# Performance work log

Measured on AMD Instinct MI355X. Metric: run time of the kernel, lower is better.

The kernel has to match this reference:

```python
import jax, jax.numpy as jnp
import numpy as np

TEMP = 0.07   # config['temperature']
EPS = 1e-8    # torch cosine-similarity eps
NEG_INF = -1e30


def _l2norm(x):
    return x / jnp.maximum(jnp.linalg.norm(x, axis=-1, keepdims=True), EPS)


def _remove_diag(m):
    # [n,n] -> [n,n-1], drop the diagonal of each row (extract_non_diagonal_matrix)
    n = m.shape[0]
    return m.reshape(-1)[:-1].reshape(n - 1, n + 1)[:, 1:].reshape(n, n - 1)


def _contrastive(e1, e2):
    # NT-Xent between two views, compared across the batch at matched temporal
    # positions (finegrain=False path). e1, e2: [b, s, d]
    b = e1.shape[0]
    z = jnp.concatenate([e1.transpose(1, 0, 2), e2.transpose(1, 0, 2)], axis=1)  # [s, 2b, d]
    zn = _l2norm(z)
    sim = jnp.einsum('pnd,pmd->pnm', zn, zn) / TEMP  # [s, 2b, 2b]
    pos = jnp.concatenate([
        jnp.diagonal(sim, b, axis1=-2, axis2=-1),
        jnp.diagonal(sim, -b, axis1=-2, axis2=-1),
    ], axis=1)  # [s, 2b]
    N = 2 * b
    eyeb = jnp.eye(b, dtype=bool)
    excl = jnp.eye(N, dtype=bool)
    excl = excl.at[:b, b:].set(excl[:b, b:] | eyeb).at[b:, :b].set(excl[b:, :b] | eyeb)
    neg = jnp.where(~excl, sim, NEG_INF)  # [s, 2b, 2b], 2b-2 live entries/row
    logits = jnp.concatenate([pos[..., None], neg], axis=-1)
    # CrossEntropyLoss(label=0), mean
    return jnp.mean(jax.nn.logsumexp(logits, axis=-1) - pos)


def _coarse_temporal(f):
    # samples within a sequence = positives, other sequences = negatives
    b, s, d = f.shape
    zn = _l2norm(f.reshape(b * s, d))
    sim = (zn @ zn.T) / TEMP  # [bs, bs]
    # diagonal over the batch blocks -> [b, s, s]
    sim_ii = jnp.diagonal(sim.reshape(b, s, b, s), axis1=0, axis2=2).transpose(2, 0, 1)
    pos = jax.vmap(_remove_diag)(sim_ii).reshape(b * s, s - 1)
    blk = jnp.repeat(jnp.repeat(~jnp.eye(b, dtype=bool), s, axis=0), s, axis=1)
    neg = jnp.where(blk, sim, NEG_INF)  # (b-1)*s live entries per row
    logits = jnp.concatenate([pos, neg], axis=1)
    return jnp.mean(jax.nn.logsumexp(logits, axis=1) - logits[:, 0])


def _ortho(x1, x2):
    # CosineEmbeddingLoss with target=-1, margin=0: mean(relu(cos(x1, x2)))
    a = _l2norm(x1.reshape(-1, x1.shape[-1]))
    b = _l2norm(x2.reshape(-1, x2.shape[-1]))
    return jnp.mean(jax.nn.relu(jnp.sum(a * b, axis=-1)))


def _forward(mod1_v1, mod1_v2, mod2_v1, mod2_v2, seq_len):
    d = mod1_v1.shape[-1]
    h = d // 2
    f1 = [mod1_v1.reshape(-1, seq_len, d), mod2_v1.reshape(-1, seq_len, d)]  # view 1, per mod
    f2 = [mod1_v2.reshape(-1, seq_len, d), mod2_v2.reshape(-1, seq_len, d)]  # view 2, per mod
    sh = lambda x: x[..., :h]
    pv = lambda x: x[..., h:]

    # (2) shared contrastive between modalities, per view
    shared_loss = _contrastive(sh(f1[0]), sh(f1[1])) + _contrastive(sh(f2[0]), sh(f2[1]))
    # (3) private contrastive between views, per modality
    private_loss = _contrastive(pv(f1[0]), pv(f2[0])) + _contrastive(pv(f1[1]), pv(f2[1]))
    # (4) orthogonality: shared-vs-private per mod per view, private-vs-private per view
    ortho_loss = (_ortho(sh(f1[0]), pv(f1[0])) + _ortho(sh(f1[1]), pv(f1[1]))
                  + _ortho(sh(f2[0]), pv(f2[0])) + _ortho(sh(f2[1]), pv(f2[1]))
                  + _ortho(pv(f1[0]), pv(f1[1])) + _ortho(pv(f2[0]), pv(f2[1])))
    # (5) temporal consistency: coarse temporal contrastive per mod per view
    temporal_loss = (_coarse_temporal(f1[0]) + _coarse_temporal(f1[1])
                     + _coarse_temporal(f2[0]) + _coarse_temporal(f2[1]))
    return shared_loss + private_loss + ortho_loss + temporal_loss


def setup_inputs() -> dict:
    key = jax.random.key(0)
    ks = jax.random.split(key, 4)
    B, S, D = 512, 8, 128
    return {
        'mod1_v1': jax.random.normal(ks[0], (B * S, D), dtype=jnp.float32),
        'mod1_v2': jax.random.normal(ks[1], (B * S, D), dtype=jnp.float32),
        'mod2_v1': jax.random.normal(ks[2], (B * S, D), dtype=jnp.float32),
        'mod2_v2': jax.random.normal(ks[3], (B * S, D), dtype=jnp.float32),
        'seq_len': S,
    }


def reference(mod1_v1, mod1_v2, mod2_v1, mod2_v2, seq_len):
    return _forward(mod1_v1, mod1_v2, mod2_v1, mod2_v2, seq_len)
```

## Files before the change

kernel.cpp:

```cpp
#include <hip/hip_runtime.h>
#include <math.h>

#define CTR_L1 0
#define CTR_L2 2048
#define RS_T   49152
#define RS_C   65536
#define SLOT   98304
#define ZF_BYTE 397312
#define ZH_BYTE 4591616

#define INV_T 14.285714285714286f
#define C1EXP 20.609929155556627f
#define EPS_N 1e-8f
#define NBLK_TAIL 192

typedef __attribute__((ext_vector_type(8))) short short8;
typedef __attribute__((ext_vector_type(4))) float floatx4;

__device__ __forceinline__ const float* pick4(const float* a, const float* b,
                                              const float* c, const float* d, int i) {
    return i == 0 ? a : i == 1 ? b : i == 2 ? c : d;
}

__device__ __forceinline__ unsigned short f2bf(float x) {
    unsigned u = __float_as_uint(x);
    u += 0x7fff + ((u >> 16) & 1);
    return (unsigned short)(u >> 16);
}

__device__ __forceinline__ ushort4 cvt4(float4 x, float sc) {
    ushort4 o;
    o.x = f2bf(x.x * sc); o.y = f2bf(x.y * sc); o.z = f2bf(x.z * sc); o.w = f2bf(x.w * sc);
    return o;
}

__global__ __launch_bounds__(256) void k_prep(const float* __restrict__ in0, const float* __restrict__ in1,
                                              const float* __restrict__ in2, const float* __restrict__ in3,
                                              float* __restrict__ ws) {
    __shared__ float ivf[128], ivs[128], ivp[128];
    __shared__ float buf[4][8][128];
    __shared__ float iv[3][32];
    __shared__ float red[3];
    const int tid = threadIdx.x;
    const int blk = blockIdx.x;

    if (blk < 128) {
        const int input = blk >> 5, g = blk & 31;
        const float* src = pick4(in0, in1, in2, in3, input) + (size_t)(g * 128) * 128;
        {
            int r = tid >> 1, half = tid & 1;
            const float* rp_ = src + r * 128 + half * 64;
            float ss = 0.0f;
            #pragma unroll
            for (int k = 0; k < 16; k++) {
                float4 x = *(const float4*)(rp_ + k * 4);
                ss = fmaf(x.x, x.x, fmaf(x.y, x.y, fmaf(x.z, x.z, fmaf(x.w, x.w, ss))));
            }
            float other = __shfl_xor(ss, 1);
            if (half == 0) {
                ivs[r] = 1.0f / fmaxf(sqrtf(ss), EPS_N);
                ivf[r] = 1.0f / fmaxf(sqrtf(ss + other), EPS_N);
            } else {
                ivp[r] = 1.0f / fmaxf(sqrtf(ss), EPS_N);
            }
        }
        __syncthreads();
        unsigned short* zf = (unsigned short*)((char*)ws + ZF_BYTE) + (size_t)input * 524288 + (size_t)g * 16384;
        unsigned short* zh = (unsigned short*)((char*)ws + ZH_BYTE) + (size_t)input * 524288;
        #pragma unroll
        for (int k = 0; k < 8; k++) {
            int ch = k * 256 + tid;
            int lr = ((ch >> 8) << 4) | (ch & 15);
            int kc = (ch >> 4) & 15;
            const float* sp = src + lr * 128 + kc * 8;
            float sc = ivf[lr];
            *(ushort4*)(zf + ch * 8)     = cvt4(*(const float4*)sp, sc);
            *(ushort4*)(zf + ch * 8 + 4) = cvt4(*(const float4*)(sp + 4), sc);
        }
        #pragma unroll
        for (int k = 0; k < 8; k++) {
            int ch = k * 256 + tid;
            int p = ch >> 8, kc = (ch >> 4) & 15, slot = ch & 15;
            int lr = slot * 8 + p;
            const float* sp = src + lr * 128 + kc * 8;
            float sc = (kc < 8 ? ivs : ivp)[lr];
            unsigned short* dst = zh + (size_t)p * 65536 + (size_t)g * 2048 + (ch & 255) * 8;
            *(ushort4*)dst       = cvt4(*(const float4*)sp, sc);
            *(ushort4*)(dst + 4) = cvt4(*(const float4*)(sp + 4), sc);
        }
        return;
    }

    const int s = blk - 128;
    int gid = s * 256 + tid;
    if (gid < 2080) ws[gid] = 0.0f;
    if (gid < 50176) ws[RS_T + gid] = 0.0f;
    if (tid < 3) red[tid] = 0.0f;

    #pragma unroll
    for (int i = 0; i < 4; i++) {
        int e4 = tid + i * 256;
        int inp = e4 >> 8, row = (e4 >> 5) & 7, c4 = e4 & 31;
        float4 f = *(const float4*)(pick4(in0, in1, in2, in3, inp) + (size_t)(s * 8 + row) * 128 + c4 * 4);
        *(float4*)(&buf[inp][row][c4 * 4]) = f;
    }
    __syncthreads();
    {
        int row32 = tid >> 3, seg = tid & 7;
        const float* rp_ = &buf[row32 >> 3][row32 & 7][seg * 16];
        float ss = 0.0f;
        #pragma unroll
        for (int k = 0; k < 4; k++) {
            float4 x = *(const float4*)(rp_ + k * 4);
            ss = fmaf(x.x, x.x, fmaf(x.y, x.y, fmaf(x.z, x.z, fmaf(x.w, x.w, ss))));
        }
        ss += __shfl_xor(ss, 1); ss += __shfl_xor(ss, 2);
        float cross = __shfl_xor(ss, 4);
        if (seg == 0) {
            iv[0][row32] = 1.0f / fmaxf(sqrtf(ss), EPS_N);
            iv[2][row32] = 1.0f / fmaxf(sqrtf(ss + cross), EPS_N);
        }
        if (seg == 4) iv[1][row32] = 1.0f / fmaxf(sqrtf(ss), EPS_N);
    }
    __syncthreads();

    float val = 0.0f;
    int cat = -1;
    if (tid < 48) {
        const int oa[6]  = {0, 2, 1, 3, 0, 1};
        const int oaf[6] = {0, 0, 0, 0, 64, 64};
        const int ob[6]  = {0, 2, 1, 3, 2, 3};
        int term = tid >> 3, row = tid & 7;
        const float* A = &buf[oa[term]][row][oaf[term]];
        const float* B = &buf[ob[term]][row][64];
        float d = 0.0f;
        #pragma unroll
        for (int k = 0; k < 16; k++) {
            float4 x = *(const float4*)(A + k * 4);
            float4 y = *(const float4*)(B + k * 4);
            d = fmaf(x.x, y.x, fmaf(x.y, y.y, fmaf(x.z, y.z, fmaf(x.w, y.w, d))));
        }
        float ia = iv[oaf[term] ? 1 : 0][oa[term] * 8 + row];
        float ib = iv[1][ob[term] * 8 + row];
        val = fmaxf(d * ia * ib, 0.0f);
        cat = 2;
    } else if (tid < 80) {
        const int ca[4] = {0, 1, 0, 2}, cb[4] = {2, 3, 1, 3}, coff[4] = {0, 0, 64, 64};
        int call = (tid - 48) >> 3, row = (tid - 48) & 7;
        const float* A = &buf[ca[call]][row][coff[call]];
        const float* B = &buf[cb[call]][row][coff[call]];
        float d = 0.0f;
        #pragma unroll
        for (int k = 0; k < 16; k++) {
            float4 x = *(const float4*)(A + k * 4);
            float4 y = *(const float4*)(B + k * 4);
            d = fmaf(x.x, y.x, fmaf(x.y, y.y, fmaf(x.z, y.z, fmaf(x.w, y.w, d))));
        }
        int ivb = coff[call] ? 1 : 0;
        val = d * iv[ivb][ca[call] * 8 + row] * iv[ivb][cb[call] * 8 + row];
        cat = 0;
    } else if (tid < 136) {
        int u = tid - 80;
        int inp = u / 14, v = u % 14, pp = v >> 1, half = v & 1;
        int ra = (pp == 0) ? 1 : (pp + 1);
        const float* A = &buf[inp][ra][half * 64];
        const float* B = &buf[inp][0][half * 64];
        float d = 0.0f;
        #pragma unroll
        for (int k = 0; k < 16; k++) {
            float4 x = *(const float4*)(A + k * 4);
            float4 y = *(const float4*)(B + k * 4);
            d = fmaf(x.x, y.x, fmaf(x.y, y.y, fmaf(x.z, y.z, fmaf(x.w, y.w, d))));
        }
        float wgt = (pp == 0) ? 2.0f : 1.0f;
        val = d * wgt * iv[2][inp * 8 + ra] * iv[2][inp * 8];
        cat = 1;
    }
    if (cat >= 0) atomicAdd(&red[cat], val);
    __syncthreads();
    if (tid == 0) atomicAdd(ws + SLOT + 32 * 24, red[0]);
    if (tid == 1) atomicAdd(ws + SLOT + 32 * 25, red[1]);
    if (tid == 2) atomicAdd(ws + SLOT + 32 * (16 + (s & 7)), red[2]);
}

__global__ __launch_bounds__(256, 3) void k_gram(float* __restrict__ ws) {
    const int tid = threadIdx.x;
    const int b = blockIdx.x;
    const int w = tid >> 6, lane = tid & 63, quad = (tid >> 4) & 3, l15 = tid & 15;
    const int wrow = (w >> 1) * 64, wcol = (w & 1) * 64;
    const int laneoff = (lane >> 4) * 128 + (lane & 15) * 8;

    const short* aPtr;
    const short* planeA;
    const short* planeB;
    int nk, ntiles, jbase, modm;
    float* rsR;
    float* rsCbase;
    bool temporal = (b < 1024);
    int rt;

    if (temporal) {
        int input = b >> 8;
        rt = (b >> 3) & 31;
        int chunk = b & 7;
        const short* zf = (const short*)((const char*)ws + ZF_BYTE) + (size_t)input * 524288;
        planeA = planeB = zf;
        aPtr = zf + (rt * 8 + (wrow >> 4)) * 2048 + laneoff;
        nk = 2; modm = 31;
        jbase = chunk * 2;
        ntiles = 2 + ((chunk == 7 && rt < 16) ? 1 : 0);
        rsR = ws + RS_T + input * 4096 + rt * 128;
        rsCbase = ws + RS_T + input * 4096;
    } else {
        int c = b - 1024;
        int call = c >> 6, p = (c >> 3) & 7;
        rt = c & 7;
        const int ca[4] = {0, 1, 0, 2}, cb[4] = {2, 3, 1, 3};
        const int hb = (call >= 2) ? 8 : 0;
        const short* zh = (const short*)((const char*)ws + ZH_BYTE);
        planeA = zh + (size_t)ca[call] * 524288 + (size_t)p * 65536 + hb * 128;
        planeB = zh + (size_t)cb[call] * 524288 + (size_t)p * 65536 + hb * 128;
        const short* rpl = (rt < 4) ? planeA : planeB;
        aPtr = rpl + ((rt & 3) * 8 + (wrow >> 4)) * 2048 + laneoff;
        nk = 1; modm = 7;
        jbase = 0;
        ntiles = (rt < 4) ? 5 : 4;
        rsR = ws + RS_C + (call * 8 + p) * 1024 + rt * 128;
        rsCbase = ws + RS_C + (call * 8 + p) * 1024;
    }

    float rp_acc[16];
    #pragma unroll
    for (int i = 0; i < 16; i++) rp_acc[i] = 0.0f;

    for (int t = 0; t < ntiles; t++) {
        int j = (temporal && t == 2) ? 16 : (jbase + t);
        int ct = (rt + j) & modm;
        bool diag = (j == 0);
        const short* bPtr;
        if (temporal) {
            bPtr = planeA + (ct * 8 + (wcol >> 4)) * 2048 + laneoff;
        } else {
            const short* cpl = (ct < 4) ? planeA : planeB;
            bPtr = cpl + ((ct & 3) * 8 + (wcol >> 4)) * 2048 + laneoff;
        }

        floatx4 acc[4][4];
        #pragma unroll
        for (int ri = 0; ri < 4; ri++)
            #pragma unroll
            for (int ci = 0; ci < 4; ci++) acc[ri][ci] = (floatx4){0.f, 0.f, 0.f, 0.f};

        for (int ksb = 0; ksb < 2 * nk; ksb++) {
            const int koff = ksb * 512;
            short8 a[4], bb[4];
            #pragma unroll
            for (int i = 0; i < 4; i++) {
                a[i]  = *(const short8*)(aPtr + i * 2048 + koff);
                bb[i] = *(const short8*)(bPtr + i * 2048 + koff);
            }
            #pragma unroll
            for (int ri = 0; ri < 4; ri++)
                #pragma unroll
                for (int ci = 0; ci < 4; ci++)
                    acc[ri][ci] = __builtin_amdgcn_mfma_f32_16x16x32_bf16(a[ri], bb[ci], acc[ri][ci], 0, 0, 0);
        }

        if (diag) {
            #pragma unroll
            for (int ri = 0; ri < 4; ri++) {
                #pragma unroll
                for (int reg = 0; reg < 4; reg++) {
                    int rloc = wrow + ri * 16 + quad * 4 + reg;
                    float rp = 0.f;
                    #pragma unroll
                    for (int ci = 0; ci < 4; ci++) {
                        int cloc = wcol + ci * 16 + l15;
                        float ex = __builtin_amdgcn_exp2f(fmaf(acc[ri][ci][reg], C1EXP, -C1EXP));
                        rp += (cloc != rloc) ? ex : 0.f;
                    }
                    rp_acc[ri * 4 + reg] += rp;
                }
            }
        } else {
            float colp[4] = {0.f, 0.f, 0.f, 0.f};
            #pragma unroll
            for (int ri = 0; ri < 4; ri++) {
                #pragma unroll
                for (int reg = 0; reg < 4; reg++) {
                    float rp = 0.f;
                    #pragma unroll
                    for (int ci = 0; ci < 4; ci++) {
                        float ex = __builtin_amdgcn_exp2f(fmaf(acc[ri][ci][reg], C1EXP, -C1EXP));
                        rp += ex;
                        colp[ci] += ex;
                    }
                    rp_acc[ri * 4 + reg] += rp;
                }
            }
            float* rsC = rsCbase + ct * 128;
            #pragma unroll
            for (int ci = 0; ci < 4; ci++) {
                colp[ci] += __shfl_xor(colp[ci], 16);
                colp[ci] += __shfl_xor(colp[ci], 32);
                if (lane < 16) atomicAdd(rsC + wcol + ci * 16 + l15, colp[ci]);
            }
        }
    }

    #pragma unroll
    for (int ri = 0; ri < 4; ri++) {
        #pragma unroll
        for (int reg = 0; reg < 4; reg++) {
            float rp = rp_acc[ri * 4 + reg];
            rp += __shfl_xor(rp, 1); rp += __shfl_xor(rp, 2);
            rp += __shfl_xor(rp, 4); rp += __shfl_xor(rp, 8);
            if (l15 == 0) atomicAdd(rsR + wrow + ri * 16 + quad * 4 + reg, rp);
        }
    }
}

__global__ __launch_bounds__(256) void k_tail(float* __restrict__ ws, float* __restrict__ out) {
    __shared__ float tred[4];
    __shared__ int lastf;
    const int tid = threadIdx.x;
    const int b = blockIdx.x;
    const int idx = b * 256 + tid;

    float l = __logf(ws[RS_T + idx]);
    #pragma unroll
    for (int m = 1; m < 64; m <<= 1) l += __shfl_xor(l, m);
    if ((tid & 63) == 0) tred[tid >> 6] = l;
    __syncthreads();
    if (tid == 0) {
        float bs = tred[0] + tred[1] + tred[2] + tred[3];
        int slot = (idx < 16384) ? (8 + (b & 7)) : (b & 7);
        atomicAdd(ws + SLOT + 32 * slot, bs);
    }
    __syncthreads();
    if (tid == 0) {
        int last = 0;
        int o1 = __hip_atomic_fetch_add((int*)(ws + CTR_L1 + 32 * (b & 7)), 1,
                                        __ATOMIC_RELAXED, __HIP_MEMORY_SCOPE_AGENT);
        if (o1 == 23) {
            int o2 = __hip_atomic_fetch_add((int*)(ws + CTR_L2), 1,
                                            __ATOMIC_RELAXED, __HIP_MEMORY_SCOPE_AGENT);
            last = (o2 == 7);
        }
        lastf = last;
    }
    __syncthreads();
    if (!lastf) return;

    if (tid < 64) {
        float v2 = 0.0f;
        if (tid < 26) {
            float x = __hip_atomic_load(ws + SLOT + 32 * tid, __ATOMIC_RELAXED, __HIP_MEMORY_SCOPE_AGENT);
            float wgt;
            if (tid < 8)       wgt = 1.0f / 8192.0f;
            else if (tid < 24) wgt = 1.0f / 4096.0f;
            else if (tid == 24) wgt = -2.0f * INV_T / 8192.0f;
            else                wgt = -INV_T / 4096.0f;
            v2 = x * wgt;
        }
        #pragma unroll
        for (int m = 1; m < 64; m <<= 1) v2 += __shfl_xor(v2, m);
        if (tid == 0) out[0] = v2 + 8.0f * INV_T;
    }
}

extern "C" void kernel_launch(void* const* d_in, const int* in_sizes, int n_in,
                              void* d_out, int out_size, void* d_ws, size_t ws_size,
                              hipStream_t stream) {
    (void)in_sizes; (void)n_in; (void)out_size; (void)ws_size;
    const float* in0 = (const float*)d_in[0];
    const float* in1 = (const float*)d_in[1];
    const float* in2 = (const float*)d_in[2];
    const float* in3 = (const float*)d_in[3];
    float* ws = (float*)d_ws;
    float* out = (float*)d_out;

    hipLaunchKernelGGL(k_prep, dim3(640), dim3(256), 0, stream, in0, in1, in2, in3, ws);
    hipLaunchKernelGGL(k_gram, dim3(1280), dim3(256), 0, stream, ws);
    hipLaunchKernelGGL(k_tail, dim3(NBLK_TAIL), dim3(256), 0, stream, ws, out);
}
```

Baseline: 114.3 us.

## Keep A fragments in registers and give each temporal block twice as many tiles

```diff
diff --git a/kernel.cpp b/kernel.cpp
--- a/kernel.cpp
+++ b/kernel.cpp
@@ -190,133 +190,188 @@
     const int wrow = (w >> 1) * 64, wcol = (w & 1) * 64;
     const int laneoff = (lane >> 4) * 128 + (lane & 15) * 8;
 
-    const short* aPtr;
-    const short* planeA;
-    const short* planeB;
-    int nk, ntiles, jbase, modm;
-    float* rsR;
-    float* rsCbase;
-    bool temporal = (b < 1024);
-    int rt;
-
-    if (temporal) {
-        int input = b >> 8;
-        rt = (b >> 3) & 31;
-        int chunk = b & 7;
+    float rp_acc[16];
+    #pragma unroll
+    for (int i = 0; i < 16; i++) rp_acc[i] = 0.0f;
+
+    if (b < 512) {
+        const int input = b >> 7, rt = (b >> 2) & 31, chunk = b & 3;
         const short* zf = (const short*)((const char*)ws + ZF_BYTE) + (size_t)input * 524288;
-        planeA = planeB = zf;
-        aPtr = zf + (rt * 8 + (wrow >> 4)) * 2048 + laneoff;
-        nk = 2; modm = 31;
-        jbase = chunk * 2;
-        ntiles = 2 + ((chunk == 7 && rt < 16) ? 1 : 0);
-        rsR = ws + RS_T + input * 4096 + rt * 128;
-        rsCbase = ws + RS_T + input * 4096;
+        const short* aPtr = zf + (rt * 8 + (wrow >> 4)) * 2048 + laneoff;
+        float* rsR = ws + RS_T + input * 4096 + rt * 128;
+        float* rsCbase = ws + RS_T + input * 4096;
+
+        short8 A[16];
+        #pragma unroll
+        for (int ksb = 0; ksb < 4; ksb++)
+            #pragma unroll
+            for (int i = 0; i < 4; i++)
+                A[ksb * 4 + i] = *(const short8*)(aPtr + i * 2048 + ksb * 512);
+
+        const int ntiles = 4 + ((chunk == 3 && rt < 16) ? 1 : 0);
+        for (int t = 0; t < ntiles; t++) {
+            int j = (t == 4) ? 16 : (chunk * 4 + t);
+            int ct = (rt + j) & 31;
+            const short* bPtr = zf + (ct * 8 + (wcol >> 4)) * 2048 + laneoff;
+
+            floatx4 acc[4][4];
+            #pragma unroll
+            for (int ri = 0; ri < 4; ri++)
+                #pragma unroll
+                for (int ci = 0; ci < 4; ci++) acc[ri][ci] = (floatx4){0.f, 0.f, 0.f, 0.f};
+
+            #pragma unroll
+            for (int ksb = 0; ksb < 4; ksb++) {
+                short8 bb[4];
+                #pragma unroll
+                for (int i = 0; i < 4; i++) bb[i] = *(const short8*)(bPtr + i * 2048 + ksb * 512);
+                #pragma unroll
+                for (int ri = 0; ri < 4; ri++)
+                    #pragma unroll
+                    for (int ci = 0; ci < 4; ci++)
+                        acc[ri][ci] = __builtin_amdgcn_mfma_f32_16x16x32_bf16(A[ksb * 4 + ri], bb[ci], acc[ri][ci], 0, 0, 0);
+            }
+
+            if (j == 0) {
+                #pragma unroll
+                for (int ri = 0; ri < 4; ri++)
+                    #pragma unroll
+                    for (int reg = 0; reg < 4; reg++) {
+                        int rloc = wrow + ri * 16 + quad * 4 + reg;
+                        float rp = 0.f;
+                        #pragma unroll
+                        for (int ci = 0; ci < 4; ci++) {
+                            int cloc = wcol + ci * 16 + l15;
+                            float ex = __builtin_amdgcn_exp2f(fmaf(acc[ri][ci][reg], C1EXP, -C1EXP));
+                            rp += (cloc != rloc) ? ex : 0.f;
+                        }
+                        rp_acc[ri * 4 + reg] += rp;
+                    }
+            } else {
+                float colp[4] = {0.f, 0.f, 0.f, 0.f};
+                #pragma unroll
+                for (int ri = 0; ri < 4; ri++)
+                    #pragma unroll
+                    for (int reg = 0; reg < 4; reg++) {
+                        float rp = 0.f;
+                        #pragma unroll
+                        for (int ci = 0; ci < 4; ci++) {
+                            float ex = __builtin_amdgcn_exp2f(fmaf(acc[ri][ci][reg], C1EXP, -C1EXP));
+                            rp += ex;
+                            colp[ci] += ex;
+                        }
+                        rp_acc[ri * 4 + reg] += rp;
+                    }
+                float* rsC = rsCbase + ct * 128;
+                #pragma unroll
+                for (int ci = 0; ci < 4; ci++) {
+                    colp[ci] += __shfl_xor(colp[ci], 16);
+                    colp[ci] += __shfl_xor(colp[ci], 32);
+                    if (lane < 16) atomicAdd(rsC + wcol + ci * 16 + l15, colp[ci]);
+                }
+            }
+        }
+        #pragma unroll
+        for (int ri = 0; ri < 4; ri++)
+            #pragma unroll
+            for (int reg = 0; reg < 4; reg++) {
+                float rp = rp_acc[ri * 4 + reg];
+                rp += __shfl_xor(rp, 1); rp += __shfl_xor(rp, 2);
+                rp += __shfl_xor(rp, 4); rp += __shfl_xor(rp, 8);
+                if (l15 == 0) atomicAdd(rsR + wrow + ri * 16 + quad * 4 + reg, rp);
+            }
     } else {
-        int c = b - 1024;
-        int call = c >> 6, p = (c >> 3) & 7;
-        rt = c & 7;
+        const int c = b - 512;
+        const int call = c >> 6, p = (c >> 3) & 7, rt = c & 7;
         const int ca[4] = {0, 1, 0, 2}, cb[4] = {2, 3, 1, 3};
         const int hb = (call >= 2) ? 8 : 0;
         const short* zh = (const short*)((const char*)ws + ZH_BYTE);
-        planeA = zh + (size_t)ca[call] * 524288 + (size_t)p * 65536 + hb * 128;
-        planeB = zh + (size_t)cb[call] * 524288 + (size_t)p * 65536 + hb * 128;
+        const short* planeA = zh + (size_t)ca[call] * 524288 + (size_t)p * 65536 + hb * 128;
+        const short* planeB = zh + (size_t)cb[call] * 524288 + (size_t)p * 65536 + hb * 128;
         const short* rpl = (rt < 4) ? planeA : planeB;
-        aPtr = rpl + ((rt & 3) * 8 + (wrow >> 4)) * 2048 + laneoff;
-        nk = 1; modm = 7;
-        jbase = 0;
-        ntiles = (rt < 4) ? 5 : 4;
-        rsR = ws + RS_C + (call * 8 + p) * 1024 + rt * 128;
-        rsCbase = ws + RS_C + (call * 8 + p) * 1024;
-    }
-
-    float rp_acc[16];
-    #pragma unroll
-    for (int i = 0; i < 16; i++) rp_acc[i] = 0.0f;
-
-    for (int t = 0; t < ntiles; t++) {
-        int j = (temporal && t == 2) ? 16 : (jbase + t);
-        int ct = (rt + j) & modm;
-        bool diag = (j == 0);
-        const short* bPtr;
-        if (temporal) {
-            bPtr = planeA + (ct * 8 + (wcol >> 4)) * 2048 + laneoff;
-        } else {
+        const short* aPtr = rpl + ((rt & 3) * 8 + (wrow >> 4)) * 2048 + laneoff;
+        float* rsR = ws + RS_C + (call * 8 + p) * 1024 + rt * 128;
+        float* rsCbase = ws + RS_C + (call * 8 + p) * 1024;
+
+        short8 A[8];
+        #pragma unroll
+        for (int ksb = 0; ksb < 2; ksb++)
+            #pragma unroll
+            for (int i = 0; i < 4; i++)
+                A[ksb * 4 + i] = *(const short8*)(aPtr + i * 2048 + ksb * 512);
+
+        const int ntiles = 4 + ((rt < 4) ? 1 : 0);
+        for (int t = 0; t < ntiles; t++) {
+            int ct = (rt + t) & 7;
             const short* cpl = (ct < 4) ? planeA : planeB;
-            bPtr = cpl + ((ct & 3) * 8 + (wcol >> 4)) * 2048 + laneoff;
-        }
-
-        floatx4 acc[4][4];
+            const short* bPtr = cpl + ((ct & 3) * 8 + (wcol >> 4)) * 2048 + laneoff;
+
+            floatx4 acc[4][4];
+            #pragma unroll
+            for (int ri = 0; ri < 4; ri++)
+                #pragma unroll
+                for (int ci = 0; ci < 4; ci++) acc[ri][ci] = (floatx4){0.f, 0.f, 0.f, 0.f};
+
+            #pragma unroll
+            for (int ksb = 0; ksb < 2; ksb++) {
+                short8 bb[4];
+                #pragma unroll
+                for (int i = 0; i < 4; i++) bb[i] = *(const short8*)(bPtr + i * 2048 + ksb * 512);
+                #pragma unroll
+                for (int ri = 0; ri < 4; ri++)
+                    #pragma unroll
+                    for (int ci = 0; ci < 4; ci++)
+                        acc[ri][ci] = __builtin_amdgcn_mfma_f32_16x16x32_bf16(A[ksb * 4 + ri], bb[ci], acc[ri][ci], 0, 0, 0);
+            }
+
+            if (t == 0) {
+                #pragma unroll
+                for (int ri = 0; ri < 4; ri++)
+                    #pragma unroll
+                    for (int reg = 0; reg < 4; reg++) {
+                        int rloc = wrow + ri * 16 + quad * 4 + reg;
+                        float rp = 0.f;
+                        #pragma unroll
+                        for (int ci = 0; ci < 4; ci++) {
+                            int cloc = wcol + ci * 16 + l15;
+                            float ex = __builtin_amdgcn_exp2f(fmaf(acc[ri][ci][reg], C1EXP, -C1EXP));
+                            rp += (cloc != rloc) ? ex : 0.f;
+                        }
+                        rp_acc[ri * 4 + reg] += rp;
+                    }
+            } else {
+                float colp[4] = {0.f, 0.f, 0.f, 0.f};
+                #pragma unroll
+                for (int ri = 0; ri < 4; ri++)
+                    #pragma unroll
+                    for (int reg = 0; reg < 4; reg++) {
+                        float rp = 0.f;
+                        #pragma unroll
+                        for (int ci = 0; ci < 4; ci++) {
+                            float ex = __builtin_amdgcn_exp2f(fmaf(acc[ri][ci][reg], C1EXP, -C1EXP));
+                            rp += ex;
+                            colp[ci] += ex;
+                        }
+                        rp_acc[ri * 4 + reg] += rp;
+                    }
+                float* rsC = rsCbase + ct * 128;
+                #pragma unroll
+                for (int ci = 0; ci < 4; ci++) {
+                    colp[ci] += __shfl_xor(colp[ci], 16);
+                    colp[ci] += __shfl_xor(colp[ci], 32);
+                    if (lane < 16) atomicAdd(rsC + wcol + ci * 16 + l15, colp[ci]);
+                }
+            }
+        }
         #pragma unroll
         for (int ri = 0; ri < 4; ri++)
             #pragma unroll
-            for (int ci = 0; ci < 4; ci++) acc[ri][ci] = (floatx4){0.f, 0.f, 0.f, 0.f};
-
-        for (int ksb = 0; ksb < 2 * nk; ksb++) {
-            const int koff = ksb * 512;
-            short8 a[4], bb[4];
-            #pragma unroll
-            for (int i = 0; i < 4; i++) {
-                a[i]  = *(const short8*)(aPtr + i * 2048 + koff);
-                bb[i] = *(const short8*)(bPtr + i * 2048 + koff);
-            }
-            #pragma unroll
-            for (int ri = 0; ri < 4; ri++)
-                #pragma unroll
-                for (int ci = 0; ci < 4; ci++)
-                    acc[ri][ci] = __builtin_amdgcn_mfma_f32_16x16x32_bf16(a[ri], bb[ci], acc[ri][ci], 0, 0, 0);
-        }
-
-        if (diag) {
-            #pragma unroll
-            for (int ri = 0; ri < 4; ri++) {
-                #pragma unroll
-                for (int reg = 0; reg < 4; reg++) {
-                    int rloc = wrow + ri * 16 + quad * 4 + reg;
-                    float rp = 0.f;
-                    #pragma unroll
-                    for (int ci = 0; ci < 4; ci++) {
-                        int cloc = wcol + ci * 16 + l15;
-                        float ex = __builtin_amdgcn_exp2f(fmaf(acc[ri][ci][reg], C1EXP, -C1EXP));
-                        rp += (cloc != rloc) ? ex : 0.f;
-                    }
-                    rp_acc[ri * 4 + reg] += rp;
-                }
-            }
-        } else {
-            float colp[4] = {0.f, 0.f, 0.f, 0.f};
-            #pragma unroll
-            for (int ri = 0; ri < 4; ri++) {
-                #pragma unroll
-                for (int reg = 0; reg < 4; reg++) {
-                    float rp = 0.f;
-                    #pragma unroll
-                    for (int ci = 0; ci < 4; ci++) {
-                        float ex = __builtin_amdgcn_exp2f(fmaf(acc[ri][ci][reg], C1EXP, -C1EXP));
-                        rp += ex;
-                        colp[ci] += ex;
-                    }
-                    rp_acc[ri * 4 + reg] += rp;
-                }
-            }
-            float* rsC = rsCbase + ct * 128;
-            #pragma unroll
-            for (int ci = 0; ci < 4; ci++) {
-                colp[ci] += __shfl_xor(colp[ci], 16);
-                colp[ci] += __shfl_xor(colp[ci], 32);
-                if (lane < 16) atomicAdd(rsC + wcol + ci * 16 + l15, colp[ci]);
-            }
-        }
-    }
-
-    #pragma unroll
-    for (int ri = 0; ri < 4; ri++) {
-        #pragma unroll
-        for (int reg = 0; reg < 4; reg++) {
-            float rp = rp_acc[ri * 4 + reg];
-            rp += __shfl_xor(rp, 1); rp += __shfl_xor(rp, 2);
-            rp += __shfl_xor(rp, 4); rp += __shfl_xor(rp, 8);
-            if (l15 == 0) atomicAdd(rsR + wrow + ri * 16 + quad * 4 + reg, rp);
-        }
+            for (int reg = 0; reg < 4; reg++) {
+                float rp = rp_acc[ri * 4 + reg];
+                rp += __shfl_xor(rp, 1); rp += __shfl_xor(rp, 2);
+                rp += __shfl_xor(rp, 4); rp += __shfl_xor(rp, 8);
+                if (l15 == 0) atomicAdd(rsR + wrow + ri * 16 + quad * 4 + reg, rp);
+            }
     }
 }
 
@@ -381,6 +436,6 @@
     float* out = (float*)d_out;
 
     hipLaunchKernelGGL(k_prep, dim3(640), dim3(256), 0, stream, in0, in1, in2, in3, ws);
-    hipLaunchKernelGGL(k_gram, dim3(1280), dim3(256), 0, stream, ws);
+    hipLaunchKernelGGL(k_gram, dim3(768), dim3(256), 0, stream, ws);
     hipLaunchKernelGGL(k_tail, dim3(NBLK_TAIL), dim3(256), 0, stream, ws, out);
 }
```

After: 124.4 us. +8.9%, slower.

## Quantize normalized embeddings to FP8 e4m3 and use FP8 MFMA for Gram tiles

Applied to the files above, without the earlier changes.

```diff
diff --git a/kernel.cpp b/kernel.cpp
--- a/kernel.cpp
+++ b/kernel.cpp
@@ -7,14 +7,13 @@
 #define RS_C   65536
 #define SLOT   98304
 #define ZF_BYTE 397312
-#define ZH_BYTE 4591616
+#define ZH8_BYTE 2494464
 
 #define INV_T 14.285714285714286f
 #define C1EXP 20.609929155556627f
 #define EPS_N 1e-8f
 #define NBLK_TAIL 192
 
-typedef __attribute__((ext_vector_type(8))) short short8;
 typedef __attribute__((ext_vector_type(4))) float floatx4;
 
 __device__ __forceinline__ const float* pick4(const float* a, const float* b,
@@ -22,16 +21,24 @@
     return i == 0 ? a : i == 1 ? b : i == 2 ? c : d;
 }
 
-__device__ __forceinline__ unsigned short f2bf(float x) {
+__device__ __forceinline__ unsigned f2e4m3(float x) {
     unsigned u = __float_as_uint(x);
-    u += 0x7fff + ((u >> 16) & 1);
-    return (unsigned short)(u >> 16);
-}
-
-__device__ __forceinline__ ushort4 cvt4(float4 x, float sc) {
-    ushort4 o;
-    o.x = f2bf(x.x * sc); o.y = f2bf(x.y * sc); o.z = f2bf(x.z * sc); o.w = f2bf(x.w * sc);
-    return o;
+    unsigned s = (u >> 24) & 0x80;
+    u &= 0x7fffffffu;
+    if (u >= 0x43e00000u) return s | 0x7e;
+    if (u < 0x3c800000u) {
+        int m = (int)rintf(__uint_as_float(u) * 512.0f);
+        return s | (unsigned)m;
+    }
+    unsigned r = u + 0x7ffffu + ((u >> 20) & 1u);
+    int e = (int)((r >> 23) & 0xffu) - 127;
+    if (e > 8) return s | 0x7e;
+    return s | (unsigned)(((e + 7) << 3) | ((r >> 20) & 7u));
+}
+
+__device__ __forceinline__ unsigned pack4_e4m3(const float* p, float sc) {
+    return f2e4m3(p[0] * sc) | (f2e4m3(p[1] * sc) << 8)
+         | (f2e4m3(p[2] * sc) << 16) | (f2e4m3(p[3] * sc) << 24);
 }
 
 __global__ __launch_bounds__(256) void k_prep(const float* __restrict__ in0, const float* __restrict__ in1,
@@ -65,28 +72,34 @@
             }
         }
         __syncthreads();
-        unsigned short* zf = (unsigned short*)((char*)ws + ZF_BYTE) + (size_t)input * 524288 + (size_t)g * 16384;
-        unsigned short* zh = (unsigned short*)((char*)ws + ZH_BYTE) + (size_t)input * 524288;
-        #pragma unroll
-        for (int k = 0; k < 8; k++) {
-            int ch = k * 256 + tid;
-            int lr = ((ch >> 8) << 4) | (ch & 15);
-            int kc = (ch >> 4) & 15;
-            const float* sp = src + lr * 128 + kc * 8;
+
+        unsigned char* zf8 = (unsigned char*)ws + ZF_BYTE + (size_t)input * 524288 + (size_t)g * 16384;
+        unsigned char* zh8 = (unsigned char*)ws + ZH8_BYTE + (size_t)input * 524288;
+        #pragma unroll
+        for (int it = 0; it < 4; it++) {
+            int ch = it * 256 + tid;
+            int gg = ch >> 7, p = (ch >> 6) & 1, q = (ch >> 4) & 3, slot = ch & 15;
+            int lr = gg * 16 + slot;
+            int k0 = p * 64 + q * 8;
+            const float* sp = src + lr * 128 + k0;
             float sc = ivf[lr];
-            *(ushort4*)(zf + ch * 8)     = cvt4(*(const float4*)sp, sc);
-            *(ushort4*)(zf + ch * 8 + 4) = cvt4(*(const float4*)(sp + 4), sc);
-        }
-        #pragma unroll
-        for (int k = 0; k < 8; k++) {
-            int ch = k * 256 + tid;
-            int p = ch >> 8, kc = (ch >> 4) & 15, slot = ch & 15;
-            int lr = slot * 8 + p;
-            const float* sp = src + lr * 128 + kc * 8;
-            float sc = (kc < 8 ? ivs : ivp)[lr];
-            unsigned short* dst = zh + (size_t)p * 65536 + (size_t)g * 2048 + (ch & 255) * 8;
-            *(ushort4*)dst       = cvt4(*(const float4*)sp, sc);
-            *(ushort4*)(dst + 4) = cvt4(*(const float4*)(sp + 4), sc);
+            int4 v;
+            v.x = (int)pack4_e4m3(sp, sc);      v.y = (int)pack4_e4m3(sp + 4, sc);
+            v.z = (int)pack4_e4m3(sp + 32, sc); v.w = (int)pack4_e4m3(sp + 36, sc);
+            *(int4*)(zf8 + (size_t)ch * 16) = v;
+        }
+        #pragma unroll
+        for (int it = 0; it < 4; it++) {
+            int ch = it * 256 + tid;
+            int ps = ch >> 7, h = (ch >> 6) & 1, q = (ch >> 4) & 3, slot = ch & 15;
+            int lr = slot * 8 + ps;
+            int c0 = h * 64 + q * 8;
+            const float* sp = src + lr * 128 + c0;
+            float sc = h ? ivp[lr] : ivs[lr];
+            int4 v;
+            v.x = (int)pack4_e4m3(sp, sc);      v.y = (int)pack4_e4m3(sp + 4, sc);
+            v.z = (int)pack4_e4m3(sp + 32, sc); v.w = (int)pack4_e4m3(sp + 36, sc);
+            *(int4*)(zh8 + (size_t)ps * 65536 + (size_t)g * 2048 + (size_t)(ch & 127) * 16) = v;
         }
         return;
     }
@@ -188,12 +201,12 @@
     const int b = blockIdx.x;
     const int w = tid >> 6, lane = tid & 63, quad = (tid >> 4) & 3, l15 = tid & 15;
     const int wrow = (w >> 1) * 64, wcol = (w & 1) * 64;
-    const int laneoff = (lane >> 4) * 128 + (lane & 15) * 8;
-
-    const short* aPtr;
-    const short* planeA;
-    const short* planeB;
-    int nk, ntiles, jbase, modm;
+    const int laneoff = quad * 256 + l15 * 16;
+
+    const char* aPtr;
+    const char* planeA;
+    const char* planeB;
+    int npair, ntiles, jbase, modm, hoff;
     float* rsR;
     float* rsCbase;
     bool temporal = (b < 1024);
@@ -203,10 +216,11 @@
         int input = b >> 8;
         rt = (b >> 3) & 31;
         int chunk = b & 7;
-        const short* zf = (const short*)((const char*)ws + ZF_BYTE) + (size_t)input * 524288;
-        planeA = planeB = zf;
-        aPtr = zf + (rt * 8 + (wrow >> 4)) * 2048 + laneoff;
-        nk = 2; modm = 31;
+        const char* zf8 = (const char*)ws + ZF_BYTE + (size_t)input * 524288;
+        planeA = planeB = zf8;
+        hoff = 0;
+        aPtr = zf8 + (size_t)(rt * 8 + (wrow >> 4)) * 2048 + laneoff;
+        npair = 2; modm = 31;
         jbase = chunk * 2;
         ntiles = 2 + ((chunk == 7 && rt < 16) ? 1 : 0);
         rsR = ws + RS_T + input * 4096 + rt * 128;
@@ -216,13 +230,13 @@
         int call = c >> 6, p = (c >> 3) & 7;
         rt = c & 7;
         const int ca[4] = {0, 1, 0, 2}, cb[4] = {2, 3, 1, 3};
-        const int hb = (call >= 2) ? 8 : 0;
-        const short* zh = (const short*)((const char*)ws + ZH_BYTE);
-        planeA = zh + (size_t)ca[call] * 524288 + (size_t)p * 65536 + hb * 128;
-        planeB = zh + (size_t)cb[call] * 524288 + (size_t)p * 65536 + hb * 128;
-        const short* rpl = (rt < 4) ? planeA : planeB;
-        aPtr = rpl + ((rt & 3) * 8 + (wrow >> 4)) * 2048 + laneoff;
-        nk = 1; modm = 7;
+        hoff = (call >= 2) ? 1024 : 0;
+        const char* zh8 = (const char*)ws + ZH8_BYTE;
+        planeA = zh8 + (size_t)ca[call] * 524288 + (size_t)p * 65536;
+        planeB = zh8 + (size_t)cb[call] * 524288 + (size_t)p * 65536;
+        const char* rpl = (rt < 4) ? planeA : planeB;
+        aPtr = rpl + (size_t)((rt & 3) * 8 + (wrow >> 4)) * 2048 + hoff + laneoff;
+        npair = 1; modm = 7;
         jbase = 0;
         ntiles = (rt < 4) ? 5 : 4;
         rsR = ws + RS_C + (call * 8 + p) * 1024 + rt * 128;
@@ -237,12 +251,12 @@
         int j = (temporal && t == 2) ? 16 : (jbase + t);
         int ct = (rt + j) & modm;
         bool diag = (j == 0);
-        const short* bPtr;
+        const char* bPtr;
         if (temporal) {
-            bPtr = planeA + (ct * 8 + (wcol >> 4)) * 2048 + laneoff;
+            bPtr = planeA + (size_t)(ct * 8 + (wcol >> 4)) * 2048 + laneoff;
         } else {
-            const short* cpl = (ct < 4) ? planeA : planeB;
-            bPtr = cpl + ((ct & 3) * 8 + (wcol >> 4)) * 2048 + laneoff;
+            const char* cpl = (ct < 4) ? planeA : planeB;
+            bPtr = cpl + (size_t)((ct & 3) * 8 + (wcol >> 4)) * 2048 + hoff + laneoff;
         }
 
         floatx4 acc[4][4];
@@ -251,19 +265,23 @@
             #pragma unroll
             for (int ci = 0; ci < 4; ci++) acc[ri][ci] = (floatx4){0.f, 0.f, 0.f, 0.f};
 
-        for (int ksb = 0; ksb < 2 * nk; ksb++) {
-            const int koff = ksb * 512;
-            short8 a[4], bb[4];
+        for (int p = 0; p < npair; p++) {
+            longlong2 av[4], bv[4];
             #pragma unroll
             for (int i = 0; i < 4; i++) {
-                a[i]  = *(const short8*)(aPtr + i * 2048 + koff);
-                bb[i] = *(const short8*)(bPtr + i * 2048 + koff);
-            }
-            #pragma unroll
-            for (int ri = 0; ri < 4; ri++)
+                av[i] = *(const longlong2*)(aPtr + (size_t)i * 2048 + p * 1024);
+                bv[i] = *(const longlong2*)(bPtr + (size_t)i * 2048 + p * 1024);
+            }
+            #pragma unroll
+            for (int h = 0; h < 2; h++) {
                 #pragma unroll
-                for (int ci = 0; ci < 4; ci++)
-                    acc[ri][ci] = __builtin_amdgcn_mfma_f32_16x16x32_bf16(a[ri], bb[ci], acc[ri][ci], 0, 0, 0);
+                for (int ri = 0; ri < 4; ri++)
+                    #pragma unroll
+                    for (int ci = 0; ci < 4; ci++)
+                        acc[ri][ci] = __builtin_amdgcn_mfma_f32_16x16x32_fp8_fp8(
+                            h ? av[ri].y : av[ri].x, h ? bv[ci].y : bv[ci].x,
+                            acc[ri][ci], 0, 0, 0);
+            }
         }
 
         if (diag) {
```

Result: slower. 120.6 us (+5.5%).
